# Performance work log

Measured on AMD Instinct MI355X. Metric: run time of the kernel, lower is better.

## Reference

```python
import jax, jax.numpy as jnp
import numpy as np

B, C, H, W = 4, 64, 256, 256
WS = 8          # window size
HEADS = 4       # dim // dim_head, dim_head = 16
DH = 16         # dim_head used for scale
HID = 64        # gated conv FFN hidden (mult=1)


def conv2d(x, w, b=None, stride=1, pad=1, groups=1):
    out = jax.lax.conv_general_dilated(
        x, w, (stride, stride), [(pad, pad), (pad, pad)],
        feature_group_count=groups,
        dimension_numbers=('NCHW', 'OIHW', 'NCHW'))
    if b is not None:
        out = out + b[None, :, None, None]
    return out


def gelu(x):
    return jax.nn.gelu(x, approximate=False)  # torch F.gelu / nn.GELU default (erf)


def ln2d(x, w, b, eps=1e-6):  # LayerNorm2d: normalize over channel dim
    mu = jnp.mean(x, axis=1, keepdims=True)
    var = jnp.mean((x - mu) ** 2, axis=1, keepdims=True)
    return w[None, :, None, None] * ((x - mu) / jnp.sqrt(var + eps)) + b[None, :, None, None]


def ln_last(x, w, b, eps=1e-5):  # nn.LayerNorm over last dim
    mu = jnp.mean(x, axis=-1, keepdims=True)
    var = jnp.mean((x - mu) ** 2, axis=-1, keepdims=True)
    return w * ((x - mu) / jnp.sqrt(var + eps)) + b


def to_windows(x, w):  # b d (x w1) (y w2) -> b x y w1 w2 d
    b, c, h, ww = x.shape
    x = x.reshape(b, c, h // w, w, ww // w, w)
    return jnp.transpose(x, (0, 2, 4, 3, 5, 1))


def from_windows(x):  # b x y w1 w2 d -> b d (x w1) (y w2)
    b, nx, ny, w1, w2, c = x.shape
    return jnp.transpose(x, (0, 5, 1, 3, 2, 4)).reshape(b, c, nx * w1, ny * w2)


def setup_inputs() -> dict:
    key = jax.random.key(0)
    ks = iter(jax.random.split(key, 64))

    def rn(*shape):
        return jax.random.normal(next(ks), shape, dtype=jnp.float32) * 0.05

    d = dict(
        x=jax.random.normal(next(ks), (B, C, H, W), dtype=jnp.float32),
        norm_w=jnp.ones((C,), jnp.float32), norm_b=jnp.zeros((C,), jnp.float32),
        conv1_w=rn(C, C, 1, 1), conv1_b=jnp.zeros((C,), jnp.float32),
        conv2_w=rn(C, 2 * C, 1, 1), conv2_b=jnp.zeros((C,), jnp.float32),
        mb_w1=rn(C, C, 1, 1), mb_b1=jnp.zeros((C,), jnp.float32),
        mb_dw_w=rn(C, 1, 3, 3), mb_dw_b=jnp.zeros((C,), jnp.float32),
        se_w1=rn(16, C), se_w2=rn(C, 16),
        mb_w2=rn(C, C, 1, 1), mb_b2=jnp.zeros((C,), jnp.float32),
        ln_att_w=jnp.ones((C,), jnp.float32), ln_att_b=jnp.zeros((C,), jnp.float32),
        q1_w=rn(C // 2, C), q1_b=jnp.zeros((C // 2,), jnp.float32),
        qkv_w=rn(3 * C // 2, C // 2),
        to_out_w=rn(C // 2, C // 2),
        sr_w=rn(C, C, 3, 3), sr_b=jnp.zeros((C,), jnp.float32),
        ln_sr_w=jnp.ones((C,), jnp.float32), ln_sr_b=jnp.zeros((C,), jnp.float32),
        kv1_w=rn(C, C), kv1_b=jnp.zeros((C,), jnp.float32),
        q2_w=rn(C // 2, C), q2_b=jnp.zeros((C // 2,), jnp.float32),
        cd_w=rn(C // 2, C // 2, 3, 3), cd_b=jnp.zeros((C // 2,), jnp.float32),
        cu_w=rn(C // 2, C // 2, 3, 3), cu_b=jnp.zeros((C // 2,), jnp.float32),
        cln1_w=jnp.ones((C,), jnp.float32), cln1_b=jnp.zeros((C,), jnp.float32),
        ff1_in_w=rn(2 * HID, C, 1, 1), ff1_dw_w=rn(2 * HID, 1, 3, 3), ff1_out_w=rn(C, HID, 1, 1),
        cln2_w=jnp.ones((C,), jnp.float32), cln2_b=jnp.zeros((C,), jnp.float32),
        ca_temp=jnp.ones((HEADS, 1, 1), jnp.float32),
        ca_qkv_w=rn(3 * C, C, 1, 1), ca_dw_w=rn(3 * C, 1, 3, 3), ca_out_w=rn(C, C, 1, 1),
        cln3_w=jnp.ones((C,), jnp.float32), cln3_b=jnp.zeros((C,), jnp.float32),
        ff2_in_w=rn(2 * HID, C, 1, 1), ff2_dw_w=rn(2 * HID, 1, 3, 3), ff2_out_w=rn(C, HID, 1, 1),
    )
    return d


def reference(x, norm_w, norm_b, conv1_w, conv1_b, conv2_w, conv2_b,
              mb_w1, mb_b1, mb_dw_w, mb_dw_b, se_w1, se_w2, mb_w2, mb_b2,
              ln_att_w, ln_att_b, q1_w, q1_b, qkv_w, to_out_w,
              sr_w, sr_b, ln_sr_w, ln_sr_b, kv1_w, kv1_b, q2_w, q2_b,
              cd_w, cd_b, cu_w, cu_b,
              cln1_w, cln1_b, ff1_in_w, ff1_dw_w, ff1_out_w,
              cln2_w, cln2_b, ca_temp, ca_qkv_w, ca_dw_w, ca_out_w,
              cln3_w, cln3_b, ff2_in_w, ff2_dw_w, ff2_out_w):
    scale = DH ** -0.5
    # input norm + 1x1 conv
    y = conv2d(ln2d(x, norm_w, norm_b), conv1_w, conv1_b, pad=0)
    # ---- MBConv (expansion 1, SE, residual) ----
    r = y
    t = gelu(conv2d(y, mb_w1, mb_b1, pad=0))
    t = gelu(conv2d(t, mb_dw_w, mb_dw_b, pad=1, groups=C))
    s = jnp.mean(t, axis=(2, 3))                      # (B,C) squeeze
    s = jax.nn.sigmoid(jax.nn.silu(s @ se_w1.T) @ se_w2.T)
    y = conv2d(t * s[:, :, None, None], mb_w2, mb_b2, pad=0) + r
    # ---- windowed hybrid attention, PreNormResidual ----
    xw = to_windows(y, WS)                            # (B,nx,ny,8,8,C)
    xn = ln_last(xw, ln_att_w, ln_att_b)
    xf = from_windows(xn)                             # (B,C,H,W)
    b, c, h, w = xf.shape
    nx, ny = h // WS, w // WS
    # window self-attention branch on dim/2
    xq = jnp.einsum('bchw,oc->bohw', xf, q1_w) + q1_b[None, :, None, None]
    tw = to_windows(xq, WS).reshape(b * nx * ny, WS * WS, c // 2)
    qkv = tw @ qkv_w.T
    q, k, v = jnp.split(qkv, 3, axis=-1)

    def heads_split(t):
        return jnp.transpose(t.reshape(t.shape[0], WS * WS, HEADS, -1), (0, 2, 1, 3))

    q, k, v = heads_split(q) * scale, heads_split(k), heads_split(v)
    attn = jax.nn.softmax(jnp.einsum('bhid,bhjd->bhij', q, k), axis=-1)
    o = jnp.einsum('bhij,bhjd->bhid', attn, v)
    o = jnp.transpose(o, (0, 2, 1, 3)).reshape(b * nx * ny, WS, WS, c // 2)
    o = (o @ to_out_w.T).reshape(b, nx, ny, WS, WS, c // 2)
    # low-resolution cross-attention branch on dim/2
    iq = jnp.einsum('bchw,oc->bohw', xf, q2_w) + q2_b[None, :, None, None]
    iq = conv2d(iq, cd_w, cd_b, stride=8, pad=1)      # (B,C/2,H/8,W/8)
    qq = jnp.transpose(iq.reshape(b, h * w // 64, HEADS // 2, c // HEADS), (0, 2, 1, 3))
    x1 = conv2d(xf, sr_w, sr_b, stride=16, pad=1)     # (B,C,h16,w16)
    x1 = jnp.transpose(x1.reshape(b, c, -1), (0, 2, 1))
    x1 = gelu(ln_last(x1, ln_sr_w, ln_sr_b))
    kv = (x1 @ kv1_w.T + kv1_b).reshape(b, -1, 2, HEADS // 2, c // HEADS)
    kv = jnp.transpose(kv, (2, 0, 3, 1, 4))
    k1, v1 = kv[0], kv[1]                             # (B,2,N,16)
    a1 = jax.nn.softmax(jnp.einsum('bhid,bhjd->bhij', qq, k1) * scale, axis=-1)
    o1 = jnp.einsum('bhij,bhjd->bhid', a1, v1)        # (B,2,HW/64,16)
    o1 = jnp.transpose(o1, (0, 1, 3, 2)).reshape(b, c // 2, h // 8, w // 8)
    o1 = jnp.repeat(jnp.repeat(o1, 8, axis=2), 8, axis=3)   # nearest upsample x8
    o1 = to_windows(conv2d(o1, cu_w, cu_b, pad=1), WS)
    xw = jnp.concatenate([o, o1], axis=-1) + xw       # residual
    y = from_windows(xw)

    def gcff(z, in_w, dw_w, out_w):
        t = conv2d(conv2d(z, in_w, pad=0), dw_w, pad=1, groups=2 * HID)
        a, g = jnp.split(t, 2, axis=1)
        return conv2d(gelu(a) * g, out_w, pad=0)

    y = y + gcff(ln2d(y, cln1_w, cln1_b), ff1_in_w, ff1_dw_w, ff1_out_w)
    # ---- windowed channel (transposed) attention ----
    z = ln2d(y, cln2_w, cln2_b)
    qkv2 = conv2d(conv2d(z, ca_qkv_w, pad=0), ca_dw_w, pad=1, groups=3 * C)
    qc, kc, vc = jnp.split(qkv2, 3, axis=1)
    hp, wp = h // WS, w // WS

    def rw(t):  # b (head d) (h ph) (w pw) -> b (h w) head d (ph pw)
        t = t.reshape(b, HEADS, C // HEADS, hp, WS, wp, WS)
        return jnp.transpose(t, (0, 3, 5, 1, 2, 4, 6)).reshape(b, hp * wp, HEADS, C // HEADS, WS * WS)

    qc, kc, vc = rw(qc), rw(kc), rw(vc)
    qc = qc / jnp.clip(jnp.linalg.norm(qc, axis=-1, keepdims=True), 1e-12)
    kc = kc / jnp.clip(jnp.linalg.norm(kc, axis=-1, keepdims=True), 1e-12)
    aat = jax.nn.softmax(jnp.einsum('bnhde,bnhfe->bnhdf', qc, kc) * ca_temp, axis=-1)
    oc = jnp.einsum('bnhdf,bnhfe->bnhde', aat, vc)    # (B,Nw,head,16,64)
    oc = oc.reshape(b, hp, wp, HEADS, C // HEADS, WS, WS)
    oc = jnp.transpose(oc, (0, 3, 4, 1, 5, 2, 6)).reshape(b, C, h, w)
    y = y + conv2d(oc, ca_out_w, pad=0)
    y = y + gcff(ln2d(y, cln3_w, cln3_b), ff2_in_w, ff2_dw_w, ff2_out_w)
    # fuse branch with block input
    return conv2d(jnp.concatenate([x, y], axis=1), conv2_w, conv2_b, pad=0)
```

## Files before the change

### kernel.cpp

```cpp
#include <hip/hip_runtime.h>
#include <hip/hip_bf16.h>
#include <math.h>

typedef __hip_bfloat16 bf16;

static constexpr int B_ = 4;
static constexpr int C_ = 64;
static constexpr int H_ = 256;
static constexpr int W_ = 256;
static constexpr int P_ = H_ * W_;
static constexpr int NP_ = B_ * P_;

__device__ __forceinline__ float cvt(float x) { return x; }
__device__ __forceinline__ float cvt(bf16 x) { return __bfloat162float(x); }
__device__ __forceinline__ float geluf(float x) { return 0.5f * x * (1.0f + erff(x * 0.70710678118654752f)); }
__device__ __forceinline__ float sigm(float x) { return 1.0f / (1.0f + __expf(-x)); }

__device__ __forceinline__ float ldin(const void* p, int i, bool bf) {
    return bf ? __bfloat162float(((const bf16*)p)[i]) : ((const float*)p)[i];
}

__device__ __forceinline__ void bf2x(unsigned u, float& a, float& b) {
    a = __uint_as_float(u << 16);
    b = __uint_as_float(u & 0xffff0000u);
}

__device__ __forceinline__ int win_swz(int bid) { return (bid & 7) * 512 + (bid >> 3); }

__global__ __launch_bounds__(256) void k_detect(const unsigned int* __restrict__ x, int* __restrict__ flag) {
    __shared__ int red[256];
    int cnt = 0;
    for (int i = threadIdx.x; i < 4096; i += 256) {
        unsigned int u = x[i];
        unsigned int e = (u >> 7) & 0xFFu;
        cnt += (e >= 100u && e <= 140u) ? 1 : 0;
    }
    red[threadIdx.x] = cnt;
    __syncthreads();
    for (int s = 128; s > 0; s >>= 1) {
        if (threadIdx.x < s) red[threadIdx.x] += red[threadIdx.x + s];
        __syncthreads();
    }
    if (threadIdx.x == 0) flag[0] = (red[0] > 2048) ? 1 : 0;
}

__global__ __launch_bounds__(256) void k_head(const void* __restrict__ x,
                                              const void* __restrict__ lnw, const void* __restrict__ lnb,
                                              const void* __restrict__ w1, const void* __restrict__ b1,
                                              const void* __restrict__ w2, const void* __restrict__ b2,
                                              float* __restrict__ Y, bf16* __restrict__ T1,
                                              const int* __restrict__ dtf) {
    const bool bf = dtf[0] != 0;
    __shared__ bf16 s1[4096], s2[4096];
    __shared__ float sb1[64], sb2[64], slw[64], slb[64];
    for (int i = threadIdx.x; i < 4096; i += 256) {
        s1[i] = __float2bfloat16(ldin(w1, i, bf));
        s2[i] = __float2bfloat16(ldin(w2, i, bf));
    }
    if (threadIdx.x < 64) {
        sb1[threadIdx.x] = ldin(b1, threadIdx.x, bf);
        sb2[threadIdx.x] = ldin(b2, threadIdx.x, bf);
        slw[threadIdx.x] = ldin(lnw, threadIdx.x, bf);
        slb[threadIdx.x] = ldin(lnb, threadIdx.x, bf);
    }
    __syncthreads();
    int g = blockIdx.x * 256 + threadIdx.x;
    int bb = g >> 16, p = g & (P_ - 1);
    int base = bb * 64 * P_ + p;
    float v[64];
    float mu = 0.f;
#pragma unroll
    for (int c = 0; c < 64; ++c) { v[c] = ldin(x, base + c * P_, bf); mu += v[c]; }
    mu *= (1.0f / 64.0f);
    float var = 0.f;
#pragma unroll
    for (int c = 0; c < 64; ++c) { float d = v[c] - mu; var += d * d; }
    float inv = rsqrtf(var * (1.0f / 64.0f) + 1e-6f);
#pragma unroll
    for (int c = 0; c < 64; ++c) v[c] = (v[c] - mu) * inv * slw[c] + slb[c];
    float y[64];
    const unsigned* u1 = (const unsigned*)s1;
    for (int o = 0; o < 64; ++o) {
        float a = sb1[o];
#pragma unroll
        for (int cc = 0; cc < 32; ++cc) {
            float wa, wb;
            bf2x(u1[o * 32 + cc], wa, wb);
            a = fmaf(wa, v[2 * cc], fmaf(wb, v[2 * cc + 1], a));
        }
        y[o] = a;
        Y[base + o * P_] = a;
    }
    const unsigned* u2 = (const unsigned*)s2;
    for (int o = 0; o < 64; ++o) {
        float a = sb2[o];
#pragma unroll
        for (int cc = 0; cc < 32; ++cc) {
            float wa, wb;
            bf2x(u2[o * 32 + cc], wa, wb);
            a = fmaf(wa, y[2 * cc], fmaf(wb, y[2 * cc + 1], a));
        }
        T1[base + o * P_] = __float2bfloat16(geluf(a));
    }
}

__global__ __launch_bounds__(256) void k_ln(const float* __restrict__ in,
                                            const void* __restrict__ w,
// ... 85 lines not shown
    int tid = threadIdx.x;
    {
        const unsigned* gq = (const unsigned*)h;
        unsigned* hu = (unsigned*)hsb;
        for (int i = tid; i < 1280; i += 256) {
            int r = i >> 7, col2 = i & 127;
            int hh = h0 - 1 + r;
            unsigned v = 0u;
            if ((unsigned)hh < (unsigned)H_) v = gq[(base + hh * W_) / 2 + col2];
            hu[r * 128 + col2] = v;
        }
    }
    float w9[9];
#pragma unroll
    for (int k = 0; k < 9; ++k) w9[k] = ldin(dww, c * 9 + k, bf);
    float bv = ldin(dwb, c, bf);
    __syncthreads();
    float acc = 0.f;
#pragma unroll
    for (int k = 0; k < 8; ++k) {
        int j = tid + k * 256;
        int r = j >> 8, x = j & 255;
        float s = bv;
#pragma unroll
        for (int kh = 0; kh < 3; ++kh) {
            const bf16* row = &hsb[(r + kh) * 256];
            float vm1 = (x > 0) ? cvt(row[x - 1]) : 0.f;
            float v0 = cvt(row[x]);
            float vp1 = (x < 255) ? cvt(row[x + 1]) : 0.f;
            s = fmaf(w9[kh * 3 + 0], vm1, s);
            s = fmaf(w9[kh * 3 + 1], v0, s);
            s = fmaf(w9[kh * 3 + 2], vp1, s);
        }
        acc += geluf(s);
    }
    red[tid] = acc;
    __syncthreads();
    for (int s2 = 128; s2 > 0; s2 >>= 1) {
        if (tid < s2) red[tid] += red[tid + s2];
        __syncthreads();
    }
    if (tid == 0) part[bc * 32 + chunk] = red[0];
}

__global__ __launch_bounds__(256) void k_se(const float* __restrict__ part,
                                            const void* __restrict__ w1,
                                            const void* __restrict__ w2,
                                            float* __restrict__ sfin,
                                            const int* __restrict__ dtf) {
    const bool bf = dtf[0] != 0;
    __shared__ float ssum[256];
    __shared__ float hbuf[B_ * 16];
    int t = threadIdx.x;
    {
        float a = 0.f;
#pragma unroll
        for (int k = 0; k < 32; ++k) a += part[t * 32 + k];
        ssum[t] = a * (1.0f / P_);
    }
    __syncthreads();
    if (t < B_ * 16) {
        int bb = t >> 4, j = t & 15;
        float a = 0.f;
        for (int c = 0; c < 64; ++c) a = fmaf(ssum[bb * 64 + c], ldin(w1, j * 64 + c, bf), a);
        hbuf[t] = a * sigm(a);
    }
    __syncthreads();
    int bb = t >> 6, c = t & 63;
    float a = 0.f;
    for (int j = 0; j < 16; ++j) a = fmaf(hbuf[bb * 16 + j], ldin(w2, c * 16 + j, bf), a);
    sfin[t] = sigm(a);
}

__global__ __launch_bounds__(256) void k_mb2w(const bf16* __restrict__ h,
                                              const void* __restrict__ dww, const void* __restrict__ dwb,
                                              const void* __restrict__ w2, const void* __restrict__ b2,
                                              const float* __restrict__ sfin,
                                              float* __restrict__ Y,
                                              const int* __restrict__ dtf) {
    const bool bf = dtf[0] != 0;
    __shared__ __align__(16) bf16 hs[64 * 120];
    __shared__ __align__(16) bf16 ts[64 * 66];
    __shared__ __align__(16) bf16 sw2T[64 * 64];
    __shared__ float sdw[576], sdb[64], sb2[64], ssc[64];
    int wid = win_swz(blockIdx.x);
    int bb = wid >> 10;
    int h0 = ((wid >> 5) & 31) * 8, w0 = (wid & 31) * 8;
    int tid = threadIdx.x;
    {
        const unsigned* gq = (const unsigned*)h;
        unsigned* hsu = (unsigned*)hs;
        for (int i = tid; i < 3840; i += 256) {
            int c = i / 60, rem = i - c * 60;
            int pr = rem / 6, j = rem - pr * 6;
            int hh = h0 + pr - 1;
            int wc = w0 - 2 + 2 * j;
            unsigned v = 0u;
            if ((unsigned)hh < (unsigned)H_ && (unsigned)wc < 255u)
                v = gq[((bb * 64 + c) * P_ + hh * W_ + wc) >> 1];
            hsu[c * 60 + pr * 6 + j] = v;
        }
    }
    for (int i = tid; i < 576; i += 256) sdw[i] = ldin(dww, i, bf);
    for (int i = tid; i < 4096; i += 256) {
        int c = i >> 6, o = i & 63;
        sw2T[c * 64 + o] = __float2bfloat16(ldin(w2, o * 64 + c, bf));
    }
    if (tid < 64) {
        sdb[tid] = ldin(dwb, tid, bf);
        sb2[tid] = ldin(b2, tid, bf);
        ssc[tid] = sfin[bb * 64 + tid];
    }
    __syncthreads();
    for (int i = tid; i < 4096; i += 256) {
        int c = i >> 6, t = i & 63;
        int rt = t >> 3, ct = t & 7;
        float s = sdb[c];
#pragma unroll
        for (int kh = 0; kh < 3; ++kh)
#pragma unroll
            for (int kw = 0; kw < 3; ++kw)
                s = fmaf(sdw[c * 9 + kh * 3 + kw], cvt(hs[c * 120 + (rt + kh) * 12 + ct + kw + 1]), s);
        ts[c * 66 + t] = __float2bfloat16(geluf(s) * ssc[c]);
    }
    __syncthreads();
    int og = tid >> 4, pg = tid & 15;
    int o0 = og * 4, p0 = pg * 4;
    float acc[4][4] = {};
    const unsigned* wt = (const unsigned*)sw2T;
    const unsigned* tt = (const unsigned*)ts;
    for (int c = 0; c < 64; ++c) {
        float w0v, w1v, w2v, w3v, t0, t1, t2, t3;
        bf2x(wt[c * 32 + (o0 >> 1)], w0v, w1v);
        bf2x(wt[c * 32 + (o0 >> 1) + 1], w2v, w3v);
        bf2x(tt[c * 33 + (p0 >> 1)], t0, t1);
        bf2x(tt[c * 33 + (p0 >> 1) + 1], t2, t3);
        acc[0][0] = fmaf(w0v, t0, acc[0][0]); acc[0][1] = fmaf(w0v, t1, acc[0][1]);
        acc[0][2] = fmaf(w0v, t2, acc[0][2]); acc[0][3] = fmaf(w0v, t3, acc[0][3]);
        acc[1][0] = fmaf(w1v, t0, acc[1][0]); acc[1][1] = fmaf(w1v, t1, acc[1][1]);
        acc[1][2] = fmaf(w1v, t2, acc[1][2]); acc[1][3] = fmaf(w1v, t3, acc[1][3]);
        acc[2][0] = fmaf(w2v, t0, acc[2][0]); acc[2][1] = fmaf(w2v, t1, acc[2][1]);
        acc[2][2] = fmaf(w2v, t2, acc[2][2]); acc[2][3] = fmaf(w2v, t3, acc[2][3]);
        acc[3][0] = fmaf(w3v, t0, acc[3][0]); acc[3][1] = fmaf(w3v, t1, acc[3][1]);
        acc[3][2] = fmaf(w3v, t2, acc[3][2]); acc[3][3] = fmaf(w3v, t3, acc[3][3]);
    }
#pragma unroll
    for (int i = 0; i < 4; ++i)
#pragma unroll
        for (int j = 0; j < 4; ++j) {
            int t = p0 + j;
            int p = (h0 + (t >> 3)) * W_ + w0 + (t & 7);
            Y[(bb * 64 + o0 + i) * P_ + p] += acc[i][j] + sb2[o0 + i];
        }
}

__global__ __launch_bounds__(256) void k_wprep(const void* __restrict__ q1w, const void* __restrict__ q1b,
                                               const void* __restrict__ qkvw, const void* __restrict__ outw,
                                               bf16* __restrict__ WQT, float* __restrict__ BQ,
                                               bf16* __restrict__ OWT,
                                               const int* __restrict__ dtf) {
    const bool bf = dtf[0] != 0;
    __shared__ float sq1[32 * 64];
    __shared__ float sqk[96 * 32];
    __shared__ float sb1[32];
    int tid = threadIdx.x;
    for (int i = tid; i < 2048; i += 256) sq1[i] = ldin(q1w, i, bf);
    for (int i = tid; i < 3072; i += 256) sqk[i] = ldin(qkvw, i, bf);
    if (tid < 32) sb1[tid] = ldin(q1b, tid, bf);
    __syncthreads();
    for (int idx = tid; idx < 6144; idx += 256) {
        int o = idx % 96, c = idx / 96;
        float a = 0.f;
        for (int k = 0; k < 32; ++k) a = fmaf(sqk[o * 32 + k], sq1[k * 64 + c], a);
        if (o < 32) a *= 0.25f;
        WQT[c * 96 + o] = __float2bfloat16(a);
    }
    if (tid < 96) {
        float a = 0.f;
        for (int k = 0; k < 32; ++k) a = fmaf(sqk[tid * 32 + k], sb1[k], a);
        if (tid < 32) a *= 0.25f;
        BQ[tid] = a;
    }
    for (int idx = tid; idx < 1024; idx += 256) {
        int o = idx >> 5, c = idx & 31;
        OWT[c * 32 + o] = __float2bfloat16(ldin(outw, o * 32 + c, bf));
    }
}

__global__ __launch_bounds__(256, 4) void k_winattn(const bf16* __restrict__ xf,
                                                    const uint4* __restrict__ WQT,
                                                    const float* __restrict__ BQ,
                                                    const unsigned* __restrict__ OWT,
                                                    float* __restrict__ Y) {
    __shared__ __align__(16) char arena[35200];
    int wid = win_swz(blockIdx.x);
    int bb = wid >> 10;
    int h0 = ((wid >> 5) & 31) * 8, w0 = (wid & 31) * 8;
    int tid = threadIdx.x;
    {
        uint4* sW4 = (uint4*)arena;
        for (int i = tid; i < 768; i += 256) sW4[i] = WQT[i];
        if (tid < 96) ((float*)(arena + 12288))[tid] = BQ[tid];
#pragma unroll
        for (int k = 0; k < 2; ++k) {
            int idx = tid + k * 256;
            int c = idx >> 3, r = idx & 7;
// ... 228 lines not shown
    int bid = blockIdx.x;
    int iblk = bid & 3;
    int j = (bid >> 2) & 1;
    int bb = bid >> 3;
    __shared__ float sk[256 * 16];
    __shared__ float svv[256 * 16];
    int kbase = ((bb * 2 + j) * 256) * 16;
    for (int idx = threadIdx.x; idx < 4096; idx += 256) { sk[idx] = k1[kbase + idx]; svv[idx] = v1[kbase + idx]; }
    __syncthreads();
    int i = iblk * 256 + threadIdx.x;
    float q[16];
    int qbase = ((bb * 32 + (i >> 5)) * 32 + (i & 31)) * 32 + j * 16;
#pragma unroll
    for (int d = 0; d < 16; ++d) q[d] = iqd[qbase + d];
    float m = -1e30f, l = 0.f, o[16];
#pragma unroll
    for (int d = 0; d < 16; ++d) o[d] = 0.f;
    for (int n = 0; n < 256; ++n) {
        float s = 0.f;
#pragma unroll
        for (int d = 0; d < 16; ++d) s = fmaf(q[d], sk[n * 16 + d], s);
        s *= 0.25f;
        float mn = fmaxf(m, s);
        float corr = __expf(m - mn);
        float e = __expf(s - mn);
        l = l * corr + e;
#pragma unroll
        for (int d = 0; d < 16; ++d) o[d] = fmaf(o[d], corr, e * svv[n * 16 + d]);
        m = mn;
    }
    float r = 1.0f / l;
#pragma unroll
    for (int d = 0; d < 16; ++d)
        o1sp[((bb * 32 + j * 16 + d) * 32 + (i >> 5)) * 32 + (i & 31)] = o[d] * r;
}

__global__ __launch_bounds__(256) void k_cuconv(const float* __restrict__ o1sp,
                                                const void* __restrict__ w,
                                                const void* __restrict__ bias,
                                                float* __restrict__ Y,
                                                const int* __restrict__ dtf) {
    const bool bf = dtf[0] != 0;
    __shared__ float sw[32 * 32 * 9];
    for (int i = threadIdx.x; i < 9216; i += 256) sw[i] = ldin(w, i, bf);
    __syncthreads();
    int g = blockIdx.x * 256 + threadIdx.x;
    int bb = g >> 16;
    int p = g & 65535;
    int h = p >> 8, x = p & 255;
    float acc[32];
#pragma unroll
    for (int oc = 0; oc < 32; ++oc) acc[oc] = ldin(bias, oc, bf);
    for (int ic = 0; ic < 32; ++ic) {
        int ibase = (bb * 32 + ic) * 1024;
        float v[9];
#pragma unroll
        for (int kh = 0; kh < 3; ++kh)
#pragma unroll
            for (int kw = 0; kw < 3; ++kw) {
                int hh = h + kh - 1, ww = x + kw - 1;
                v[kh * 3 + kw] = ((unsigned)hh < (unsigned)H_ && (unsigned)ww < (unsigned)W_)
                                     ? o1sp[ibase + (hh >> 3) * 32 + (ww >> 3)] : 0.f;
            }
        for (int oc = 0; oc < 32; ++oc) {
            const float* wr = &sw[(oc * 32 + ic) * 9];
            float a = acc[oc];
#pragma unroll
            for (int k = 0; k < 9; ++k) a = fmaf(wr[k], v[k], a);
            acc[oc] = a;
        }
    }
#pragma unroll
    for (int oc = 0; oc < 32; ++oc) Y[(bb * 64 + 32 + oc) * P_ + p] += acc[oc];
}

__global__ __launch_bounds__(256) void k_gcff2(const bf16* __restrict__ mid_g,
                                               const void* __restrict__ dww,
                                               const void* __restrict__ outw,
                                               float* __restrict__ Y,
                                               const int* __restrict__ dtf) {
    const bool bf = dtf[0] != 0;
    __shared__ __align__(16) char arena[39168];
    bf16* mid = (bf16*)arena;
    bf16* ts = (bf16*)(arena + 26112);
    float* sdw = (float*)(arena + 34560);
    bf16* sowT = (bf16*)arena;
    int wid = win_swz(blockIdx.x);
    int bb = wid >> 10;
    int h0 = ((wid >> 5) & 31) * 8, w0 = (wid & 31) * 8;
    int tid = threadIdx.x;
    for (int i = tid; i < 1152; i += 256) sdw[i] = ldin(dww, i, bf);
    for (int i = tid; i < 12800; i += 256) {
        int c = i / 100, px = i - c * 100;
        int pr = px / 10, pc = px - pr * 10;
        int hh = h0 + pr - 1, ww = w0 + pc - 1;
        bf16 v = ((unsigned)hh < (unsigned)H_ && (unsigned)ww < (unsigned)W_)
                     ? mid_g[(bb * 128 + c) * P_ + hh * W_ + ww] : __float2bfloat16(0.f);
        mid[c * 102 + px] = v;
    }
    __syncthreads();
    for (int i = tid; i < 4096; i += 256) {
        int c = i >> 6, t = i & 63;
        int rt = t >> 3, ct = t & 7;
        float a = 0.f, g2 = 0.f;
#pragma unroll
        for (int kh = 0; kh < 3; ++kh)
#pragma unroll
            for (int kw = 0; kw < 3; ++kw) {
                int px = (rt + kh) * 10 + ct + kw;
                a = fmaf(sdw[c * 9 + kh * 3 + kw], cvt(mid[c * 102 + px]), a);
                g2 = fmaf(sdw[(c + 64) * 9 + kh * 3 + kw], cvt(mid[(c + 64) * 102 + px]), g2);
            }
        ts[c * 66 + t] = __float2bfloat16(geluf(a) * g2);
    }
    __syncthreads();
    for (int i = tid; i < 4096; i += 256) {
        int c = i >> 6, o = i & 63;
        sowT[c * 64 + o] = __float2bfloat16(ldin(outw, o * 64 + c, bf));
    }
    __syncthreads();
    int og = tid >> 4, pg = tid & 15;
    int o0 = og * 4, p0 = pg * 4;
    float acc[4][4] = {};
    const unsigned* wt = (const unsigned*)sowT;
    const unsigned* tt = (const unsigned*)ts;
    for (int c = 0; c < 64; ++c) {
        float w0v, w1v, w2v, w3v, t0, t1, t2, t3;
        bf2x(wt[c * 32 + (o0 >> 1)], w0v, w1v);
        bf2x(wt[c * 32 + (o0 >> 1) + 1], w2v, w3v);
        bf2x(tt[c * 33 + (p0 >> 1)], t0, t1);
        bf2x(tt[c * 33 + (p0 >> 1) + 1], t2, t3);
        acc[0][0] = fmaf(w0v, t0, acc[0][0]); acc[0][1] = fmaf(w0v, t1, acc[0][1]);
        acc[0][2] = fmaf(w0v, t2, acc[0][2]); acc[0][3] = fmaf(w0v, t3, acc[0][3]);
        acc[1][0] = fmaf(w1v, t0, acc[1][0]); acc[1][1] = fmaf(w1v, t1, acc[1][1]);
        acc[1][2] = fmaf(w1v, t2, acc[1][2]); acc[1][3] = fmaf(w1v, t3, acc[1][3]);
        acc[2][0] = fmaf(w2v, t0, acc[2][0]); acc[2][1] = fmaf(w2v, t1, acc[2][1]);
        acc[2][2] = fmaf(w2v, t2, acc[2][2]); acc[2][3] = fmaf(w2v, t3, acc[2][3]);
        acc[3][0] = fmaf(w3v, t0, acc[3][0]); acc[3][1] = fmaf(w3v, t1, acc[3][1]);
        acc[3][2] = fmaf(w3v, t2, acc[3][2]); acc[3][3] = fmaf(w3v, t3, acc[3][3]);
    }
#pragma unroll
    for (int i = 0; i < 4; ++i)
#pragma unroll
        for (int j = 0; j < 4; ++j) {
            int t = p0 + j;
            int p = (h0 + (t >> 3)) * W_ + w0 + (t & 7);
            Y[(bb * 64 + o0 + i) * P_ + p] += acc[i][j];
        }
}

__global__ __launch_bounds__(256) void k_chattn2(const bf16* __restrict__ qkv_g,
                                                 const void* __restrict__ dww,
                                                 const void* __restrict__ outw,
                                                 const void* __restrict__ tempw,
                                                 float* __restrict__ Y,
                                                 const int* __restrict__ dtf) {
    const bool bf = dtf[0] != 0;
    __shared__ __align__(16) char arena[51200];
    bf16* sq = (bf16*)arena;
    bf16* chunkb = (bf16*)(arena + 25344);
    float* sdwc = (float*)(arena + 40704);
    bf16* s_owT = (bf16*)(arena + 43008);
    float* s_att = (float*)(arena + 25344);
    bf16* s_oc = (bf16*)(arena + 29696);
    int wid = win_swz(blockIdx.x);
    int bb = wid >> 10;
    int h0 = ((wid >> 5) & 31) * 8, w0 = (wid & 31) * 8;
    int tid = threadIdx.x;
    const unsigned* gq = (const unsigned*)qkv_g;
    unsigned* cbu = (unsigned*)chunkb;
    for (int chunk = 0; chunk < 3; ++chunk) {
        int ch0 = chunk * 64;
        for (int i = tid; i < 3840; i += 256) {
            int c = i / 60, rem = i - c * 60;
            int pr = rem / 6, j = rem - pr * 6;
            int hh = h0 + pr - 1;
            int wc = w0 - 2 + 2 * j;
            unsigned v = 0u;
            if ((unsigned)hh < (unsigned)H_ && (unsigned)wc < 255u)
                v = gq[(((bb * 192 + ch0 + c) * P_) + hh * W_ + wc) >> 1];
            cbu[c * 60 + pr * 6 + j] = v;
        }
        for (int i = tid; i < 576; i += 256) sdwc[i] = ldin(dww, ch0 * 9 + i, bf);
        __syncthreads();
        for (int i = tid; i < 4096; i += 256) {
            int c = i >> 6, t = i & 63;
            int rt = t >> 3, ct = t & 7;
            float a = 0.f;
#pragma unroll
            for (int kh = 0; kh < 3; ++kh)
#pragma unroll
                for (int kw = 0; kw < 3; ++kw)
                    a = fmaf(sdwc[c * 9 + kh * 3 + kw], cvt(chunkb[c * 120 + (rt + kh) * 12 + ct + kw + 1]), a);
            sq[(ch0 + c) * 66 + t] = __float2bfloat16(a);
        }
        __syncthreads();
    }
    if (tid < 128) {
        int r = tid;
        float ss = 0.f;
        for (int t = 0; t < 64; ++t) { float v = cvt(sq[r * 66 + t]); ss = fmaf(v, v, ss); }
        float inv = 1.0f / fmaxf(sqrtf(ss), 1e-12f);
        for (int t = 0; t < 64; ++t) sq[r * 66 + t] = __float2bfloat16(cvt(sq[r * 66 + t]) * inv);
    }
    __syncthreads();
    for (int i = tid; i < 1024; i += 256) {
        int hh = i >> 8, d = (i >> 4) & 15, f = i & 15;
        float acc = 0.f;
        for (int t = 0; t < 64; ++t)
            acc = fmaf(cvt(sq[(hh * 16 + d) * 66 + t]), cvt(sq[(64 + hh * 16 + f) * 66 + t]), acc);
        s_att[(hh * 16 + d) * 17 + f] = acc * ldin(tempw, hh, bf);
    }
    __syncthreads();
    if (tid < 64) {
        int row = tid;
        float m = -1e30f;
        for (int f = 0; f < 16; ++f) m = fmaxf(m, s_att[row * 17 + f]);
        float sum = 0.f;
        for (int f = 0; f < 16; ++f) { float e = __expf(s_att[row * 17 + f] - m); s_att[row * 17 + f] = e; sum += e; }
        float r = 1.0f / sum;
        for (int f = 0; f < 16; ++f) s_att[row * 17 + f] *= r;
    }
    __syncthreads();
    for (int i = tid; i < 4096; i += 256) {
        int row = i >> 6, t = i & 63;
        int hh = row >> 4, d = row & 15;
        float acc = 0.f;
#pragma unroll
        for (int f = 0; f < 16; ++f)
            acc = fmaf(s_att[(hh * 16 + d) * 17 + f], cvt(sq[(128 + hh * 16 + f) * 66 + t]), acc);
        s_oc[row * 66 + t] = __float2bfloat16(acc);
    }
    for (int i = tid; i < 4096; i += 256) {
        int c = i >> 6, o = i & 63;
        s_owT[c * 64 + o] = __float2bfloat16(ldin(outw, o * 64 + c, bf));
    }
    __syncthreads();
    int og = tid >> 4, pg = tid & 15;
    int o0 = og * 4, p0 = pg * 4;
    float acc[4][4] = {};
    const unsigned* wt = (const unsigned*)s_owT;
    const unsigned* tt = (const unsigned*)s_oc;
    for (int c = 0; c < 64; ++c) {
        float w0v, w1v, w2v, w3v, t0, t1, t2, t3;
        bf2x(wt[c * 32 + (o0 >> 1)], w0v, w1v);
        bf2x(wt[c * 32 + (o0 >> 1) + 1], w2v, w3v);
        bf2x(tt[c * 33 + (p0 >> 1)], t0, t1);
        bf2x(tt[c * 33 + (p0 >> 1) + 1], t2, t3);
        acc[0][0] = fmaf(w0v, t0, acc[0][0]); acc[0][1] = fmaf(w0v, t1, acc[0][1]);
        acc[0][2] = fmaf(w0v, t2, acc[0][2]); acc[0][3] = fmaf(w0v, t3, acc[0][3]);
        acc[1][0] = fmaf(w1v, t0, acc[1][0]); acc[1][1] = fmaf(w1v, t1, acc[1][1]);
        acc[1][2] = fmaf(w1v, t2, acc[1][2]); acc[1][3] = fmaf(w1v, t3, acc[1][3]);
        acc[2][0] = fmaf(w2v, t0, acc[2][0]); acc[2][1] = fmaf(w2v, t1, acc[2][1]);
        acc[2][2] = fmaf(w2v, t2, acc[2][2]); acc[2][3] = fmaf(w2v, t3, acc[2][3]);
        acc[3][0] = fmaf(w3v, t0, acc[3][0]); acc[3][1] = fmaf(w3v, t1, acc[3][1]);
        acc[3][2] = fmaf(w3v, t2, acc[3][2]); acc[3][3] = fmaf(w3v, t3, acc[3][3]);
    }
#pragma unroll
    for (int i = 0; i < 4; ++i)
#pragma unroll
        for (int j = 0; j < 4; ++j) {
            int t = p0 + j;
            int p = (h0 + (t >> 3)) * W_ + w0 + (t & 7);
            Y[(bb * 64 + o0 + i) * P_ + p] += acc[i][j];
        }
}

__global__ __launch_bounds__(256) void k_final(const void* __restrict__ x,
                                               const float* __restrict__ Yb,
                                               const void* __restrict__ w,
                                               const void* __restrict__ bias,
                                               void* __restrict__ out,
                                               const int* __restrict__ dtf) {
    const bool bf = dtf[0] != 0;
    __shared__ float sw[64 * 128];
    __shared__ float sb[64];
    for (int i = threadIdx.x; i < 8192; i += 256) sw[i] = ldin(w, i, bf);
    if (threadIdx.x < 64) sb[threadIdx.x] = ldin(bias, threadIdx.x, bf);
    __syncthreads();
    int g = blockIdx.x * 256 + threadIdx.x;
    int bb = g >> 16;
    int p = g & 65535;
    float xv[64], yv[64];
    int base = bb * 64 * P_ + p;
#pragma unroll
    for (int c = 0; c < 64; ++c) xv[c] = ldin(x, base + c * P_, bf);
#pragma unroll
    for (int c = 0; c < 64; ++c) yv[c] = Yb[base + c * P_];
    for (int o = 0; o < 64; ++o) {
        float acc = sb[o];
        const float* wr = &sw[o * 128];
#pragma unroll
        for (int c = 0; c < 64; ++c) acc = fmaf(wr[c], xv[c], acc);
#pragma unroll
        for (int c = 0; c < 64; ++c) acc = fmaf(wr[64 + c], yv[c], acc);
        if (bf) ((bf16*)out)[base + o * P_] = __float2bfloat16(acc);
        else    ((float*)out)[base + o * P_] = acc;
    }
}

extern "C" void kernel_launch(void* const* d_in, const int* in_sizes, int n_in,
                              void* d_out, int out_size, void* d_ws, size_t ws_size,
                              hipStream_t stream) {
    const void* x        = d_in[0];
    const void* norm_w   = d_in[1];
    const void* norm_b   = d_in[2];
    const void* conv1_w  = d_in[3];
    const void* conv1_b  = d_in[4];
    const void* conv2_w  = d_in[5];
    const void* conv2_b  = d_in[6];
    const void* mb_w1    = d_in[7];
    const void* mb_b1    = d_in[8];
    const void* mb_dw_w  = d_in[9];
    const void* mb_dw_b  = d_in[10];
// ... 85 lines not shown
```

Baseline: 2.229 ms.

## Vectorize depthwise conv and attention shared-memory access with packed bf16 pairs

Reworks the depthwise 3x3 convolutions in the MBConv, gated FFN and channel-attention kernels. Each thread now owns one channel quarter, keeps its 9 filter weights in registers instead of shared memory, and reads packed bf16 pairs so it can compute two outputs per iteration. The attention normalization, QK and AV loops also read and write 32-bit packed pairs. The aim is fewer shared-memory loads, fewer integer divisions and less index arithmetic. The cost is higher register pressure and per-thread strided global loads in the halo-fill loops.

Measured after the change: 2.160 ms. 3.1% less time.

```diff
diff --git a/kernel.cpp b/kernel.cpp
--- a/kernel.cpp
+++ b/kernel.cpp
@@ -23,6 +23,14 @@
 __device__ __forceinline__ void bf2x(unsigned u, float& a, float& b) {
     a = __uint_as_float(u << 16);
     b = __uint_as_float(u & 0xffff0000u);
+}
+__device__ __forceinline__ float bflo(unsigned u) { return __uint_as_float(u << 16); }
+__device__ __forceinline__ float bfhi(unsigned u) { return __uint_as_float(u & 0xffff0000u); }
+__device__ __forceinline__ unsigned bfpack(float a, float b) {
+    union { unsigned u; bf16 h[2]; } pk;
+    pk.h[0] = __float2bfloat16(a);
+    pk.h[1] = __float2bfloat16(b);
+    return pk.u;
 }
 
 __device__ __forceinline__ int win_swz(int bid) { return (bid & 7) * 512 + (bid >> 3); }
@@ -274,26 +282,32 @@
     __shared__ __align__(16) bf16 hs[64 * 120];
     __shared__ __align__(16) bf16 ts[64 * 66];
     __shared__ __align__(16) bf16 sw2T[64 * 64];
-    __shared__ float sdw[576], sdb[64], sb2[64], ssc[64];
+    __shared__ float sdb[64], sb2[64], ssc[64];
     int wid = win_swz(blockIdx.x);
     int bb = wid >> 10;
     int h0 = ((wid >> 5) & 31) * 8, w0 = (wid & 31) * 8;
     int tid = threadIdx.x;
+    int cch = tid >> 2, quarter = tid & 3;
     {
         const unsigned* gq = (const unsigned*)h;
         unsigned* hsu = (unsigned*)hs;
-        for (int i = tid; i < 3840; i += 256) {
-            int c = i / 60, rem = i - c * 60;
-            int pr = rem / 6, j = rem - pr * 6;
+        int j = quarter * 15;
+        int pr = j / 6, col = j - pr * 6;
+        size_t chb = (size_t)(bb * 64 + cch) * P_;
+        for (int k = 0; k < 15; ++k) {
             int hh = h0 + pr - 1;
-            int wc = w0 - 2 + 2 * j;
+            int wcx = w0 - 2 + 2 * col;
             unsigned v = 0u;
-            if ((unsigned)hh < (unsigned)H_ && (unsigned)wc < 255u)
-                v = gq[((bb * 64 + c) * P_ + hh * W_ + wc) >> 1];
-            hsu[c * 60 + pr * 6 + j] = v;
-        }
-    }
-    for (int i = tid; i < 576; i += 256) sdw[i] = ldin(dww, i, bf);
+            if ((unsigned)hh < (unsigned)H_ && (unsigned)wcx < 255u)
+                v = gq[(chb + hh * W_ + wcx) >> 1];
+            hsu[cch * 60 + j] = v;
+            ++j; ++col;
+            if (col == 6) { col = 0; ++pr; }
+        }
+    }
+    float w9[9];
+#pragma unroll
+    for (int k = 0; k < 9; ++k) w9[k] = ldin(dww, cch * 9 + k, bf);
     for (int i = tid; i < 4096; i += 256) {
         int c = i >> 6, o = i & 63;
         sw2T[c * 64 + o] = __float2bfloat16(ldin(w2, o * 64 + c, bf));
@@ -304,16 +318,29 @@
         ssc[tid] = sfin[bb * 64 + tid];
     }
     __syncthreads();
-    for (int i = tid; i < 4096; i += 256) {
-        int c = i >> 6, t = i & 63;
-        int rt = t >> 3, ct = t & 7;
-        float s = sdb[c];
-#pragma unroll
-        for (int kh = 0; kh < 3; ++kh)
-#pragma unroll
-            for (int kw = 0; kw < 3; ++kw)
-                s = fmaf(sdw[c * 9 + kh * 3 + kw], cvt(hs[c * 120 + (rt + kh) * 12 + ct + kw + 1]), s);
-        ts[c * 66 + t] = __float2bfloat16(geluf(s) * ssc[c]);
+    {
+        const unsigned* mua = (const unsigned*)hs + cch * 60;
+        unsigned* tsu = (unsigned*)ts;
+        float bv = sdb[cch];
+        float sc = ssc[cch];
+#pragma unroll
+        for (int k = 0; k < 8; ++k) {
+            int p = quarter * 8 + k;
+            int t0 = 2 * p;
+            int rt = t0 >> 3, ct = t0 & 7;
+            float a0 = bv, a1 = bv;
+#pragma unroll
+            for (int kh = 0; kh < 3; ++kh) {
+                int rb = (rt + kh) * 6 + (ct >> 1);
+                unsigned u0 = mua[rb], u1 = mua[rb + 1], u2 = mua[rb + 2];
+                float x1 = bfhi(u0);
+                float x2 = bflo(u1), x3 = bfhi(u1);
+                float x4 = bflo(u2);
+                a0 = fmaf(w9[kh * 3 + 0], x1, fmaf(w9[kh * 3 + 1], x2, fmaf(w9[kh * 3 + 2], x3, a0)));
+                a1 = fmaf(w9[kh * 3 + 0], x2, fmaf(w9[kh * 3 + 1], x3, fmaf(w9[kh * 3 + 2], x4, a1)));
+            }
+            tsu[cch * 33 + p] = bfpack(geluf(a0) * sc, geluf(a1) * sc);
+        }
     }
     __syncthreads();
     int og = tid >> 4, pg = tid & 15;
@@ -708,36 +735,66 @@
     const bool bf = dtf[0] != 0;
     __shared__ __align__(16) char arena[39168];
     bf16* mid = (bf16*)arena;
-    bf16* ts = (bf16*)(arena + 26112);
-    float* sdw = (float*)(arena + 34560);
+    bf16* ts = (bf16*)(arena + 30720);
     bf16* sowT = (bf16*)arena;
     int wid = win_swz(blockIdx.x);
     int bb = wid >> 10;
     int h0 = ((wid >> 5) & 31) * 8, w0 = (wid & 31) * 8;
     int tid = threadIdx.x;
-    for (int i = tid; i < 1152; i += 256) sdw[i] = ldin(dww, i, bf);
-    for (int i = tid; i < 12800; i += 256) {
-        int c = i / 100, px = i - c * 100;
-        int pr = px / 10, pc = px - pr * 10;
-        int hh = h0 + pr - 1, ww = w0 + pc - 1;
-        bf16 v = ((unsigned)hh < (unsigned)H_ && (unsigned)ww < (unsigned)W_)
-                     ? mid_g[(bb * 128 + c) * P_ + hh * W_ + ww] : __float2bfloat16(0.f);
-        mid[c * 102 + px] = v;
-    }
-    __syncthreads();
-    for (int i = tid; i < 4096; i += 256) {
-        int c = i >> 6, t = i & 63;
-        int rt = t >> 3, ct = t & 7;
-        float a = 0.f, g2 = 0.f;
-#pragma unroll
-        for (int kh = 0; kh < 3; ++kh)
-#pragma unroll
-            for (int kw = 0; kw < 3; ++kw) {
-                int px = (rt + kh) * 10 + ct + kw;
-                a = fmaf(sdw[c * 9 + kh * 3 + kw], cvt(mid[c * 102 + px]), a);
-                g2 = fmaf(sdw[(c + 64) * 9 + kh * 3 + kw], cvt(mid[(c + 64) * 102 + px]), g2);
+    {
+        const unsigned* gq = (const unsigned*)mid_g;
+        unsigned* mu = (unsigned*)mid;
+        int c = tid >> 1, half = tid & 1;
+        int j = half * 30;
+        int pr = half * 5, col = 0;
+        size_t chb = (size_t)(bb * 128 + c) * P_;
+        for (int k = 0; k < 30; ++k) {
+            int hh = h0 + pr - 1;
+            int wcx = w0 - 2 + 2 * col;
+            unsigned v = 0u;
+            if ((unsigned)hh < (unsigned)H_ && (unsigned)wcx < 255u)
+                v = gq[(chb + hh * W_ + wcx) >> 1];
+            mu[c * 60 + j] = v;
+            ++j; ++col;
+            if (col == 6) { col = 0; ++pr; }
+        }
+    }
+    int cch = tid >> 2, quarter = tid & 3;
+    float wa9[9], wg9[9];
+#pragma unroll
+    for (int k = 0; k < 9; ++k) {
+        wa9[k] = ldin(dww, cch * 9 + k, bf);
+        wg9[k] = ldin(dww, (cch + 64) * 9 + k, bf);
+    }
+    __syncthreads();
+    {
+        const unsigned* mua = (const unsigned*)mid + cch * 60;
+        const unsigned* mug = (const unsigned*)mid + (cch + 64) * 60;
+        unsigned* tsu = (unsigned*)ts;
+#pragma unroll
+        for (int k = 0; k < 8; ++k) {
+            int p = quarter * 8 + k;
+            int t0 = 2 * p;
+            int rt = t0 >> 3, ct = t0 & 7;
+            float a0 = 0.f, a1 = 0.f, g0 = 0.f, g1 = 0.f;
+#pragma unroll
+            for (int kh = 0; kh < 3; ++kh) {
+                int rb = (rt + kh) * 6 + (ct >> 1);
+                unsigned ua0 = mua[rb], ua1 = mua[rb + 1], ua2 = mua[rb + 2];
+                unsigned ug0 = mug[rb], ug1 = mug[rb + 1], ug2 = mug[rb + 2];
+                float x1 = bfhi(ua0);
+                float x2 = bflo(ua1), x3 = bfhi(ua1);
+                float x4 = bflo(ua2);
+                a0 = fmaf(wa9[kh * 3 + 0], x1, fmaf(wa9[kh * 3 + 1], x2, fmaf(wa9[kh * 3 + 2], x3, a0)));
+                a1 = fmaf(wa9[kh * 3 + 0], x2, fmaf(wa9[kh * 3 + 1], x3, fmaf(wa9[kh * 3 + 2], x4, a1)));
+                float y1 = bfhi(ug0);
+                float y2 = bflo(ug1), y3 = bfhi(ug1);
+                float y4 = bflo(ug2);
+                g0 = fmaf(wg9[kh * 3 + 0], y1, fmaf(wg9[kh * 3 + 1], y2, fmaf(wg9[kh * 3 + 2], y3, g0)));
+                g1 = fmaf(wg9[kh * 3 + 0], y2, fmaf(wg9[kh * 3 + 1], y3, fmaf(wg9[kh * 3 + 2], y4, g1)));
             }
-        ts[c * 66 + t] = __float2bfloat16(geluf(a) * g2);
+            tsu[cch * 33 + p] = bfpack(geluf(a0) * g0, geluf(a1) * g1);
+        }
     }
     __syncthreads();
     for (int i = tid; i < 4096; i += 256) {
@@ -782,59 +839,92 @@
                                                  float* __restrict__ Y,
                                                  const int* __restrict__ dtf) {
     const bool bf = dtf[0] != 0;
-    __shared__ __align__(16) char arena[51200];
+    __shared__ __align__(16) char arena[48896];
     bf16* sq = (bf16*)arena;
     bf16* chunkb = (bf16*)(arena + 25344);
-    float* sdwc = (float*)(arena + 40704);
-    bf16* s_owT = (bf16*)(arena + 43008);
+    bf16* s_owT = (bf16*)(arena + 40704);
     float* s_att = (float*)(arena + 25344);
     bf16* s_oc = (bf16*)(arena + 29696);
     int wid = win_swz(blockIdx.x);
     int bb = wid >> 10;
     int h0 = ((wid >> 5) & 31) * 8, w0 = (wid & 31) * 8;
     int tid = threadIdx.x;
+    int cch = tid >> 2, quarter = tid & 3;
     const unsigned* gq = (const unsigned*)qkv_g;
     unsigned* cbu = (unsigned*)chunkb;
+    unsigned* squ = (unsigned*)sq;
+    int j0 = quarter * 15;
+    int pr0 = j0 / 6, col0 = j0 - pr0 * 6;
     for (int chunk = 0; chunk < 3; ++chunk) {
         int ch0 = chunk * 64;
-        for (int i = tid; i < 3840; i += 256) {
-            int c = i / 60, rem = i - c * 60;
-            int pr = rem / 6, j = rem - pr * 6;
-            int hh = h0 + pr - 1;
-            int wc = w0 - 2 + 2 * j;
-            unsigned v = 0u;
-            if ((unsigned)hh < (unsigned)H_ && (unsigned)wc < 255u)
-                v = gq[(((bb * 192 + ch0 + c) * P_) + hh * W_ + wc) >> 1];
-            cbu[c * 60 + pr * 6 + j] = v;
-        }
-        for (int i = tid; i < 576; i += 256) sdwc[i] = ldin(dww, ch0 * 9 + i, bf);
+        {
+            int j = j0, pr = pr0, col = col0;
+            size_t chb = (size_t)((bb * 192 + ch0 + cch) * P_);
+            for (int k = 0; k < 15; ++k) {
+                int hh = h0 + pr - 1;
+                int wcx = w0 - 2 + 2 * col;
+                unsigned v = 0u;
+                if ((unsigned)hh < (unsigned)H_ && (unsigned)wcx < 255u)
+                    v = gq[(chb + hh * W_ + wcx) >> 1];
+                cbu[cch * 60 + j] = v;
+                ++j; ++col;
+                if (col == 6) { col = 0; ++pr; }
+            }
+        }
+        float w9[9];
+#pragma unroll
+        for (int k = 0; k < 9; ++k) w9[k] = ldin(dww, (ch0 + cch) * 9 + k, bf);
         __syncthreads();
-        for (int i = tid; i < 4096; i += 256) {
-            int c = i >> 6, t = i & 63;
-            int rt = t >> 3, ct = t & 7;
-            float a = 0.f;
-#pragma unroll
-            for (int kh = 0; kh < 3; ++kh)
-#pragma unroll
-                for (int kw = 0; kw < 3; ++kw)
-                    a = fmaf(sdwc[c * 9 + kh * 3 + kw], cvt(chunkb[c * 120 + (rt + kh) * 12 + ct + kw + 1]), a);
-            sq[(ch0 + c) * 66 + t] = __float2bfloat16(a);
+        {
+            const unsigned* mua = cbu + cch * 60;
+#pragma unroll
+            for (int k = 0; k < 8; ++k) {
+                int p = quarter * 8 + k;
+                int t0 = 2 * p;
+                int rt = t0 >> 3, ct = t0 & 7;
+                float a0 = 0.f, a1 = 0.f;
+#pragma unroll
+                for (int kh = 0; kh < 3; ++kh) {
+                    int rb = (rt + kh) * 6 + (ct >> 1);
+                    unsigned u0 = mua[rb], u1 = mua[rb + 1], u2 = mua[rb + 2];
+                    float x1 = bfhi(u0);
+                    float x2 = bflo(u1), x3 = bfhi(u1);
+                    float x4 = bflo(u2);
+                    a0 = fmaf(w9[kh * 3 + 0], x1, fmaf(w9[kh * 3 + 1], x2, fmaf(w9[kh * 3 + 2], x3, a0)));
+                    a1 = fmaf(w9[kh * 3 + 0], x2, fmaf(w9[kh * 3 + 1], x3, fmaf(w9[kh * 3 + 2], x4, a1)));
+                }
+                squ[(ch0 + cch) * 33 + p] = bfpack(a0, a1);
+            }
         }
         __syncthreads();
     }
     if (tid < 128) {
-        int r = tid;
+        unsigned* row = squ + tid * 33;
+        float v[64];
         float ss = 0.f;
-        for (int t = 0; t < 64; ++t) { float v = cvt(sq[r * 66 + t]); ss = fmaf(v, v, ss); }
+#pragma unroll
+        for (int t2 = 0; t2 < 32; ++t2) {
+            bf2x(row[t2], v[2 * t2], v[2 * t2 + 1]);
+            ss = fmaf(v[2 * t2], v[2 * t2], fmaf(v[2 * t2 + 1], v[2 * t2 + 1], ss));
+        }
         float inv = 1.0f / fmaxf(sqrtf(ss), 1e-12f);
-        for (int t = 0; t < 64; ++t) sq[r * 66 + t] = __float2bfloat16(cvt(sq[r * 66 + t]) * inv);
+#pragma unroll
+        for (int t2 = 0; t2 < 32; ++t2)
+            row[t2] = bfpack(v[2 * t2] * inv, v[2 * t2 + 1] * inv);
     }
     __syncthreads();
     for (int i = tid; i < 1024; i += 256) {
         int hh = i >> 8, d = (i >> 4) & 15, f = i & 15;
+        const unsigned* qrow = squ + (hh * 16 + d) * 33;
+        const unsigned* krow = squ + (64 + hh * 16 + f) * 33;
         float acc = 0.f;
-        for (int t = 0; t < 64; ++t)
-            acc = fmaf(cvt(sq[(hh * 16 + d) * 66 + t]), cvt(sq[(64 + hh * 16 + f) * 66 + t]), acc);
+#pragma unroll
+        for (int t2 = 0; t2 < 32; ++t2) {
+            float q0, q1, k0, k1;
+            bf2x(qrow[t2], q0, q1);
+            bf2x(krow[t2], k0, k1);
+            acc = fmaf(q0, k0, fmaf(q1, k1, acc));
+        }
         s_att[(hh * 16 + d) * 17 + f] = acc * ldin(tempw, hh, bf);
     }
     __syncthreads();
@@ -848,14 +938,23 @@
         for (int f = 0; f < 16; ++f) s_att[row * 17 + f] *= r;
     }
     __syncthreads();
-    for (int i = tid; i < 4096; i += 256) {
-        int row = i >> 6, t = i & 63;
-        int hh = row >> 4, d = row & 15;
-        float acc = 0.f;
-#pragma unroll
-        for (int f = 0; f < 16; ++f)
-            acc = fmaf(s_att[(hh * 16 + d) * 17 + f], cvt(sq[(128 + hh * 16 + f) * 66 + t]), acc);
-        s_oc[row * 66 + t] = __float2bfloat16(acc);
+    {
+        unsigned* s_ocu = (unsigned*)s_oc;
+        for (int i = tid; i < 2048; i += 256) {
+            int row = i >> 5, p = i & 31;
+            int hh = row >> 4, d = row & 15;
+            const float* arow = &s_att[(hh * 16 + d) * 17];
+            float o0 = 0.f, o1 = 0.f;
+#pragma unroll
+            for (int f = 0; f < 16; ++f) {
+                float av = arow[f];
+                float v0, v1;
+                bf2x(squ[(128 + hh * 16 + f) * 33 + p], v0, v1);
+                o0 = fmaf(av, v0, o0);
+                o1 = fmaf(av, v1, o1);
+            }
+            s_ocu[row * 33 + p] = bfpack(o0, o1);
+        }
     }
     for (int i = tid; i < 4096; i += 256) {
         int c = i >> 6, o = i & 63;
```
